# Performance work log

Hardware: AMD Instinct MI355X
Metric: run time of the kernel (lower is better)

## Reference

```python
import jax, jax.numpy as jnp
import numpy as np

N, D, E = 32768, 128, 524288
B, L = 64, 512          # 64 graphs of 512 nodes
H, DH = 8, 16           # heads, head dim


def setup_inputs() -> dict:
    key = jax.random.key(0)
    ks = jax.random.split(key, 16)
    s = 0.02
    w = lambda k, shape: (jax.random.normal(k, shape, jnp.float32) * s)
    z = lambda *shape: jnp.zeros(shape, jnp.float32)
    o = lambda *shape: jnp.ones(shape, jnp.float32)
    return {
        "x": jax.random.normal(ks[0], (N, D), jnp.float32),
        "edge_index": jax.random.randint(ks[1], (2, E), 0, N, jnp.int32),
        "eps": jnp.zeros(()),
        "W_loc1": w(ks[2], (D, 2 * D)), "b_loc1": z(2 * D),
        "W_loc2": w(ks[3], (2 * D, D)), "b_loc2": z(D),
        "g1": o(D), "beta1": z(D),
        "Wq": w(ks[4], (D, D)), "bq": z(D),
        "Wk": w(ks[5], (D, D)), "bk": z(D),
        "Wv": w(ks[6], (D, D)), "bv": z(D),
        "Wo": w(ks[7], (D, D)), "bo": z(D),
        "g2": o(D), "beta2": z(D),
        "Wf1": w(ks[8], (D, 2 * D)), "bf1": z(2 * D),
        "Wf2": w(ks[9], (2 * D, D)), "bf2": z(D),
        "g3": o(D), "beta3": z(D),
    }


def _bn(x, g, b):
    # BatchNorm1d, training mode: batch stats over the node dimension
    m = x.mean(0)
    v = x.var(0)
    return (x - m) * jax.lax.rsqrt(v + 1e-5) * g + b


def reference(x, edge_index, eps, W_loc1, b_loc1, W_loc2, b_loc2, g1, beta1,
              Wq, bq, Wk, bk, Wv, bv, Wo, bo, g2, beta2,
              Wf1, bf1, Wf2, bf2, g3, beta3):
    src, dst = edge_index[0], edge_index[1]
    # --- local MPNN (GIN): sum-aggregate neighbours then MLP ---
    agg = jax.ops.segment_sum(x[src], dst, num_segments=N)          # [N, D]
    h = (1.0 + eps) * x + agg
    h = jax.nn.relu(h @ W_loc1 + b_loc1) @ W_loc2 + b_loc2
    h_local = _bn(x + h, g1, beta1)
    # --- global attention over each graph's (permuted) node sequence ---
    xd = x.reshape(B, L, D)
    q = (xd @ Wq + bq).reshape(B, L, H, DH)
    k = (xd @ Wk + bk).reshape(B, L, H, DH)
    v = (xd @ Wv + bv).reshape(B, L, H, DH)
    scores = jnp.einsum("blhd,bmhd->bhlm", q, k) / np.sqrt(DH)
    attn = jax.nn.softmax(scores, axis=-1)
    o = jnp.einsum("bhlm,bmhd->blhd", attn, v).reshape(B, L, D)
    o = (o @ Wo + bo).reshape(N, D)
    h_attn = _bn(x + o, g2, beta2)
    # --- combine + FFN block ---
    h = h_local + h_attn
    f = jax.nn.relu(h @ Wf1 + bf1) @ Wf2 + bf2
    return _bn(h + f, g3, beta3)
```

## Files before the change

### kernel.cpp

```cpp
#include <hip/hip_runtime.h>
#include <cstdint>
#include <cstddef>

typedef unsigned short u16;
typedef unsigned int u32;

using short8 = __attribute__((ext_vector_type(8))) short;
using f32x4  = __attribute__((ext_vector_type(4))) float;

__device__ __forceinline__ float b2f(u16 v) {
  union { u32 u; float f; } c; c.u = ((u32)v) << 16; return c.f;
}
__device__ __forceinline__ u16 f2b(float f) {
  union { float f; u32 u; } c; c.f = f;
  u32 u = c.u;
  u += 0x7fffu + ((u >> 16) & 1u);
  return (u16)(u >> 16);
}

__global__ __launch_bounds__(256)
void f2bf_kernel(const float* __restrict__ in, u16* __restrict__ outp) {
  int i = blockIdx.x * 256 + threadIdx.x;
  int el = i * 2;
  int m = ((el >> 11) << 4) | ((el >> 5) & 15);
  int n = (((el >> 9) & 3) << 5) | (el & 31);
  float2 v = *(const float2*)(in + (size_t)m * 128 + n);
  *(u32*)(outp + el) = (u32)f2b(v.x) | ((u32)f2b(v.y) << 16);
}

__global__ __launch_bounds__(256)
void prep_kernel(const float* __restrict__ Wl1, const float* __restrict__ Wl2,
                 const float* __restrict__ Wq,  const float* __restrict__ Wk,
                 const float* __restrict__ Wv,  const float* __restrict__ Wo,
                 const float* __restrict__ Wf1, const float* __restrict__ Wf2,
                 const float* __restrict__ bl1, const float* __restrict__ bl2,
                 const float* __restrict__ bq,  const float* __restrict__ bk,
                 const float* __restrict__ bv,  const float* __restrict__ bo,
                 const float* __restrict__ bf1, const float* __restrict__ bf2,
                 u16* __restrict__ Bt, float* __restrict__ biasAll) {
  int idx = blockIdx.x * 256 + threadIdx.x;
  if (idx < 196608) {
    const float* W; int local, K, N;
    if      (idx <  32768) { W = Wl1; local = idx;          K = 128; N = 256; }
    else if (idx <  65536) { W = Wl2; local = idx - 32768;  K = 256; N = 128; }
    else if (idx <  81920) { W = Wq;  local = idx - 65536;  K = 128; N = 128; }
    else if (idx <  98304) { W = Wk;  local = idx - 81920;  K = 128; N = 128; }
    else if (idx < 114688) { W = Wv;  local = idx - 98304;  K = 128; N = 128; }
    else if (idx < 131072) { W = Wo;  local = idx - 114688; K = 128; N = 128; }
    else if (idx < 163840) { W = Wf1; local = idx - 131072; K = 128; N = 256; }
    else                   { W = Wf2; local = idx - 163840; K = 256; N = 128; }
    int ks2 = (K == 256) ? 3 : 2;
    int tile = local >> 9, within = local & 511;
    int nr = within >> 5, kc = within & 31;
    int n = ((tile >> ks2) << 4) + nr;
    int k = ((tile & ((1 << ks2) - 1)) << 5) + kc;
    Bt[idx] = f2b(W[(size_t)k * N + n]);
  }
  int t = idx - 196608;
  if (t >= 0 && t < 1280) {
    float v;
    if      (t <  256) v = bl1[t];
    else if (t <  384) v = bl2[t - 256];
    else if (t <  512) v = bq[t - 384];
    else if (t <  640) v = bk[t - 512];
    else if (t <  768) v = bv[t - 640];
    else if (t <  896) v = bo[t - 768];
    else if (t < 1152) v = bf1[t - 896];
    else               v = bf2[t - 1152];
    biasAll[t] = v;
  }
}

__global__ void hist_kernel(const int* __restrict__ dst, int* __restrict__ deg, int E) {
  int i = blockIdx.x * 256 + threadIdx.x;
  if (i < E) atomicAdd(&deg[dst[i]], 1);
}

__global__ __launch_bounds__(256)
void scan1_kernel(const int* __restrict__ deg, int* __restrict__ bsum) {
  int t = threadIdx.x, b = blockIdx.x;
  int v = deg[b * 256 + t];
#pragma unroll
  for (int off = 1; off < 64; off <<= 1) v += __shfl_xor(v, off);
  __shared__ int wsum[4];
  if ((t & 63) == 0) wsum[t >> 6] = v;
  __syncthreads();
  if (t == 0) bsum[b] = wsum[0] + wsum[1] + wsum[2] + wsum[3];
}

__global__ void scan2_kernel(const int* __restrict__ bsum, int* __restrict__ boff,
                             int* __restrict__ rowptrN) {
  __shared__ int sh[128];
  int t = threadIdx.x;
  int v = bsum[t];
  sh[t] = v;
  __syncthreads();
  for (int off = 1; off < 128; off <<= 1) {
    int u = (t >= off) ? sh[t - off] : 0;
    __syncthreads();
    sh[t] += u;
    __syncthreads();
  }
  boff[t] = sh[t] - v;
  if (t == 127) *rowptrN = sh[127];
}

__global__ __launch_bounds__(256)
void scan3_kernel(const int* __restrict__ deg, const int* __restrict__ boff,
                  int* __restrict__ rowptr, int* __restrict__ cursor) {
  __shared__ int sh[256];
  int t = threadIdx.x, b = blockIdx.x;
  int idx = b * 256 + t;
  int v = deg[idx];
  sh[t] = v;
  __syncthreads();
  for (int off = 1; off < 256; off <<= 1) {
    int u = (t >= off) ? sh[t - off] : 0;
    __syncthreads();
    sh[t] += u;
    __syncthreads();
  }
  int ex = sh[t] - v + boff[b];
  rowptr[idx] = ex;
  cursor[idx] = ex;
}

__global__ void scatter_kernel(const int* __restrict__ src, const int* __restrict__ dst,
                               int* __restrict__ cursor, int* __restrict__ csr, int E) {
  int i = blockIdx.x * 256 + threadIdx.x;
  if (i < E) {
    int d = dst[i];
    int pos = atomicAdd(&cursor[d], 1);
    csr[pos] = src[i];
  }
}

__global__ __launch_bounds__(256)
void agg_kernel(const u16* __restrict__ xb, const float* __restrict__ x,
                const int* __restrict__ csr, const int* __restrict__ rowptr,
                const float* __restrict__ eps, u16* __restrict__ hin, int N) {
  int node = blockIdx.x * 4 + (threadIdx.x >> 6);
  if (node >= N) return;
  int lane = threadIdx.x & 63;
  int laneoff = (lane >> 4) * 512 + (lane & 15) * 2;
  float ep1 = 1.0f + eps[0];
  int s0 = rowptr[node], s1 = rowptr[node + 1];
  float a0 = 0.f, a1 = 0.f;
  int e = s0;
  for (; e + 4 <= s1; e += 4) {
    int i0 = csr[e], i1 = csr[e + 1], i2 = csr[e + 2], i3 = csr[e + 3];
    u32 w0 = *(const u32*)(xb + (size_t)(i0 >> 4) * 2048 + (i0 & 15) * 32 + laneoff);
    u32 w1 = *(const u32*)(xb + (size_t)(i1 >> 4) * 2048 + (i1 & 15) * 32 + laneoff);
    u32 w2 = *(const u32*)(xb + (size_t)(i2 >> 4) * 2048 + (i2 & 15) * 32 + laneoff);
    u32 w3 = *(const u32*)(xb + (size_t)(i3 >> 4) * 2048 + (i3 & 15) * 32 + laneoff);
    a0 += b2f((u16)w0) + b2f((u16)w1) + b2f((u16)w2) + b2f((u16)w3);
    a1 += b2f((u16)(w0 >> 16)) + b2f((u16)(w1 >> 16))
        + b2f((u16)(w2 >> 16)) + b2f((u16)(w3 >> 16));
  }
  for (; e < s1; e++) {
    int s = csr[e];
    u32 w = *(const u32*)(xb + (size_t)(s >> 4) * 2048 + (s & 15) * 32 + laneoff);
    a0 += b2f((u16)w);
    a1 += b2f((u16)(w >> 16));
  }
  float2 xw = *(const float2*)(x + (size_t)node * 128 + lane * 2);
  a0 += ep1 * xw.x;
  a1 += ep1 * xw.y;
  *(u32*)(hin + (size_t)(node >> 4) * 2048 + (node & 15) * 32 + laneoff)
      = (u32)f2b(a0) | ((u32)f2b(a1) << 16);
}

template<int K>
__global__ __launch_bounds__(256)
void gemm_fast(const u16* __restrict__ A, const u16* __restrict__ Bt,
               const float* __restrict__ bias, const u16* __restrict__ residb,
               u16* __restrict__ C0, u16* __restrict__ C1, u16* __restrict__ C2,
               float* __restrict__ ssum, float* __restrict__ ssq,
               int ntshift, int relu, float scale0, int headmajor) {
  const int tid = threadIdx.x, wave = tid >> 6, lane = tid & 63;
  const int quad = lane >> 4, c = lane & 15;
  const int y = blockIdx.y;
  const int ti = y >> ntshift, ntv = y & ((1 << ntshift) - 1);
  const int Nout = 32 << ntshift;
  const int nc32 = Nout >> 5;
  constexpr int KT = K >> 5;
  const u16* Btp = Bt + (size_t)ti * Nout * K;
  const float* bp = bias + ti * Nout;
  u16* C = (ti == 0) ? C0 : ((ti == 1) ? C1 : C2);
  const float scl = (ti == 0) ? scale0 : 1.0f;
  const int row0 = blockIdx.x * 128 + wave * 32;
  const int mt0 = row0 >> 4;
  const int col0 = ntv * 32;
  const int loff = c * 32 + quad * 8;

  const u16* Ap0 = A   + (size_t)(mt0)     * KT * 512 + loff;
  const u16* Ap1 = A   + (size_t)(mt0 + 1) * KT * 512 + loff;
  const u16* Bp0 = Btp + (size_t)(ntv * 2)     * KT * 512 + loff;
  const u16* Bp1 = Btp + (size_t)(ntv * 2 + 1) * KT * 512 + loff;

  f32x4 acc[2][2];
#pragma unroll
  for (int i = 0; i < 2; i++)
#pragma unroll
    for (int j = 0; j < 2; j++)
#pragma unroll
      for (int r = 0; r < 4; r++) acc[i][j][r] = 0.f;

#pragma unroll
  for (int i = 0; i < KT; i++) {
    short8 a0 = *(const short8*)(Ap0 + i * 512);
    short8 a1 = *(const short8*)(Ap1 + i * 512);
    short8 b0 = *(const short8*)(Bp0 + i * 512);
    short8 b1 = *(const short8*)(Bp1 + i * 512);
    acc[0][0] = __builtin_amdgcn_mfma_f32_16x16x32_bf16(a0, b0, acc[0][0], 0, 0, 0);
    acc[0][1] = __builtin_amdgcn_mfma_f32_16x16x32_bf16(a0, b1, acc[0][1], 0, 0, 0);
    acc[1][0] = __builtin_amdgcn_mfma_f32_16x16x32_bf16(a1, b0, acc[1][0], 0, 0, 0);
    acc[1][1] = __builtin_amdgcn_mfma_f32_16x16x32_bf16(a1, b1, acc[1][1], 0, 0, 0);
  }

#pragma unroll
  for (int ci = 0; ci < 2; ci++) {
    int col = col0 + ci * 16 + c;
    float bv = bp[col];
    float sp = 0.f, qp = 0.f;
#pragma unroll
    for (int mi = 0; mi < 2; mi++) {
#pragma unroll
      for (int r = 0; r < 4; r++) {
        int m = row0 + mi * 16 + quad * 4 + r;
        float v = acc[mi][ci][r] + bv;
        if (relu) v = fmaxf(v, 0.f);
        if (residb)
          v += b2f(residb[((size_t)(mt0 + mi) * 4 + (col >> 5)) * 512
                          + (quad * 4 + r) * 32 + (col & 31)]);
        v *= scl;
        size_t cidx;
        if (headmajor) {
          int bb = m >> 9, j = m & 511;
          cidx = (size_t)(bb * 8 + (col >> 4)) * 8192 + (size_t)j * 16 + (col & 15);
        } else {
          cidx = ((size_t)(mt0 + mi) * nc32 + ntv) * 512
               + (quad * 4 + r) * 32 + ci * 16 + c;
        }
        C[cidx] = f2b(v);
        sp += v; qp += v * v;
      }
    }
    if (ssum) {
      sp += __shfl_xor(sp, 16); sp += __shfl_xor(sp, 32);
      qp += __shfl_xor(qp, 16); qp += __shfl_xor(qp, 32);
      if (quad == 0) {
        atomicAdd(&ssum[col], sp);
        atomicAdd(&ssq[col], qp);
      }
    }
  }
}

__global__ __launch_bounds__(512)
void attn_kernel(const u16* __restrict__ Q, const u16* __restrict__ Km,
                 const u16* __restrict__ Vm, u16* __restrict__ O) {
  __shared__ __align__(16) u16 Vt[16 * 520];
  __shared__ __align__(16) u16 Psh[8][16 * 40];
  const int bh = blockIdx.x >> 1, qhalf = blockIdx.x & 1;
  const int b = bh >> 3, hh = bh & 7;
  const size_t qkvbase = (size_t)bh * 8192;
  const int tid = threadIdx.x;

  {
    int g = tid >> 5, i = (tid >> 1) & 15, dh = tid & 1;
    int jA = g * 32 + i;
    const u16* vp = Vm + qkvbase + (size_t)jA * 16 + dh * 8;
    short8 rowA = *(const short8*)(vp);
    short8 rowB = *(const short8*)(vp + 256);
    int j2 = g * 32 + 2 * i;
#pragma unroll
    for (int d = 0; d < 8; d++)
      *(u32*)&Vt[(dh * 8 + d) * 520 + j2] =
          (u32)(u16)rowA[d] | ((u32)(u16)rowB[d] << 16);
  }
  __syncthreads();

  const int wave = tid >> 6, lane = tid & 63;
  const int quad = lane >> 4, c = lane & 15;
  u16* Pw = &Psh[wave][0];
  u32* Pw32 = (u32*)Pw;

  short8 ones;
#pragma unroll
  for (int i = 0; i < 8; i++) ones[i] = (short)0x3F80;
  const f32x4 zero = {0.f, 0.f, 0.f, 0.f};

  short8 qf[2] = {(short8)0, (short8)0};
#pragma unroll
  for (int t = 0; t < 2; t++) {
    int qt = qhalf * 16 + wave + t * 8;
    if (quad < 2)
      qf[t] = *(const short8*)(Q + qkvbase + (size_t)(qt * 16 + c) * 16 + quad * 8);
  }

#pragma unroll
  for (int t = 0; t < 2; t++) {
    const int qt = qhalf * 16 + wave + t * 8;
    f32x4 accO = zero, accL = zero;
#pragma unroll 4
    for (int jp = 0; jp < 16; jp++) {
      short8 kf0 = (short8)0, kf1 = (short8)0;
      if (quad < 2) {
        kf0 = *(const short8*)(Km + qkvbase + (size_t)(jp * 32 + c) * 16 + quad * 8);
        kf1 = *(const short8*)(Km + qkvbase + (size_t)(jp * 32 + 16 + c) * 16 + quad * 8);
      }
      f32x4 s0 = __builtin_amdgcn_mfma_f32_16x16x32_bf16(qf[t], kf0, zero, 0, 0, 0);
      f32x4 s1 = __builtin_amdgcn_mfma_f32_16x16x32_bf16(qf[t], kf1, zero, 0, 0, 0);
#pragma unroll
      for (int r = 0; r < 4; r++) {
        union { float f; u32 u; } u0, u1;
        u0.f = exp2f(s0[r]);
        u1.f = exp2f(s1[r]);
        Pw32[(quad * 4 + r) * 20 + c] = (u0.u >> 16) | (u1.u & 0xffff0000u);
      }
      short8 pf = *(const short8*)&Pw[c * 40 + quad * 8];
      short8 vf = *(const short8*)&Vt[c * 520 + jp * 32 + quad * 8];
      accO = __builtin_amdgcn_mfma_f32_16x16x32_bf16(pf, vf, accO, 0, 0, 0);
      accL = __builtin_amdgcn_mfma_f32_16x16x32_bf16(pf, ones, accL, 0, 0, 0);
    }
#pragma unroll
    for (int r = 0; r < 4; r++) {
      float o = accO[r] / accL[r];
      size_t oidx = ((size_t)(b * 32 + qt) * 4 + (hh >> 1)) * 512
                  + (quad * 4 + r) * 32 + (hh & 1) * 16 + c;
      O[oidx] = f2b(o);
    }
  }
}

__global__ __launch_bounds__(256)
void combine_kernel(const u16* __restrict__ y1, const u16* __restrict__ y2,
                    const float* __restrict__ stats,
                    const float* __restrict__ g1, const float* __restrict__ be1,
                    const float* __restrict__ g2, const float* __restrict__ be2,
                    u16* __restrict__ hout, float invM) {
  int i = blockIdx.x * 256 + threadIdx.x;
  int e0 = i * 2;
  int c = (((e0 >> 9) & 3) << 5) | (e0 & 31);
  float sc1a, sh1a, sc1b, sh1b, sc2a, sh2a, sc2b, sh2b;
  {
    float m = stats[c] * invM, vv = stats[128 + c] * invM - m * m;
    sc1a = g1[c] * rsqrtf(vv + 1e-5f); sh1a = be1[c] - m * sc1a;
    m = stats[c + 1] * invM; vv = stats[129 + c] * invM - m * m;
    sc1b = g1[c + 1] * rsqrtf(vv + 1e-5f); sh1b = be1[c + 1] - m * sc1b;
    m = stats[256 + c] * invM; vv = stats[384 + c] * invM - m * m;
    sc2a = g2[c] * rsqrtf(vv + 1e-5f); sh2a = be2[c] - m * sc2a;
    m = stats[257 + c] * invM; vv = stats[385 + c] * invM - m * m;
    sc2b = g2[c + 1] * rsqrtf(vv + 1e-5f); sh2b = be2[c + 1] - m * sc2b;
  }
  u32 w1 = *(const u32*)(y1 + e0);
  u32 w2 = *(const u32*)(y2 + e0);
  float r0 = b2f((u16)w1) * sc1a + sh1a + b2f((u16)w2) * sc2a + sh2a;
  float r1 = b2f((u16)(w1 >> 16)) * sc1b + sh1b + b2f((u16)(w2 >> 16)) * sc2b + sh2b;
  *(u32*)(hout + e0) = (u32)f2b(r0) | ((u32)f2b(r1) << 16);
}

__global__ __launch_bounds__(256)
void norm_kernel(const u16* __restrict__ y3, const float* __restrict__ stats3,
                 const float* __restrict__ g3, const float* __restrict__ be3,
                 float* __restrict__ outp, float invM) {
  int i = blockIdx.x * 256 + threadIdx.x;
  int e0 = i * 2;
  int m = ((e0 >> 11) << 4) | ((e0 >> 5) & 15);
  int c = (((e0 >> 9) & 3) << 5) | (e0 & 31);
  float mm = stats3[c] * invM, vv = stats3[128 + c] * invM - mm * mm;
  float sca = g3[c] * rsqrtf(vv + 1e-5f), sha = be3[c] - mm * sca;
  mm = stats3[c + 1] * invM; vv = stats3[129 + c] * invM - mm * mm;
  float scb = g3[c + 1] * rsqrtf(vv + 1e-5f), shb = be3[c + 1] - mm * scb;
  u32 w = *(const u32*)(y3 + e0);
  float2 r;
  r.x = b2f((u16)w) * sca + sha;
  r.y = b2f((u16)(w >> 16)) * scb + shb;
  *(float2*)(outp + (size_t)m * 128 + c) = r;
}

extern "C" void kernel_launch(void* const* d_in, const int* in_sizes, int n_in,
                              void* d_out, int out_size, void* d_ws, size_t ws_size,
                              hipStream_t stream) {
  const float* x   = (const float*)d_in[0];
  const int*   ei  = (const int*)d_in[1];
  const float* eps = (const float*)d_in[2];
  const float* Wl1 = (const float*)d_in[3];  const float* bl1 = (const float*)d_in[4];
  const float* Wl2 = (const float*)d_in[5];  const float* bl2 = (const float*)d_in[6];
  const float* g1  = (const float*)d_in[7];  const float* be1 = (const float*)d_in[8];
  const float* Wq  = (const float*)d_in[9];  const float* bq  = (const float*)d_in[10];
  const float* Wk  = (const float*)d_in[11]; const float* bk  = (const float*)d_in[12];
  const float* Wv  = (const float*)d_in[13]; const float* bv  = (const float*)d_in[14];
  const float* Wo  = (const float*)d_in[15]; const float* bo  = (const float*)d_in[16];
  const float* g2  = (const float*)d_in[17]; const float* be2 = (const float*)d_in[18];
  const float* Wf1 = (const float*)d_in[19]; const float* bf1 = (const float*)d_in[20];
  const float* Wf2 = (const float*)d_in[21]; const float* bf2 = (const float*)d_in[22];
  const float* g3  = (const float*)d_in[23]; const float* be3 = (const float*)d_in[24];
  float* out = (float*)d_out;

  const int N = in_sizes[0] / 128;
  const int E = in_sizes[1] / 2;
  const size_t MB = 1048576;
  const float invM = 1.0f / (float)N;

  char* ws = (char*)d_ws;
  u16* hin = (u16*)(ws + 0);
  u16* t1  = (u16*)(ws + 8 * MB);
  int* deg    = (int*)(ws + 8 * MB);
  int* rowptr = (int*)(ws + 8 * MB + 256 * 1024);
  int* cursor = (int*)(ws + 8 * MB + 512 * 1024);
  int* csr    = (int*)(ws + 8 * MB + 768 * 1024);
  u16* qb  = (u16*)(ws + 24 * MB);
  u16* kb  = (u16*)(ws + 32 * MB);
  u16* vb  = (u16*)(ws + 40 * MB);
  u16* xb  = (u16*)(ws + 48 * MB);
  u16* y2  = xb;
  float* stats = (float*)(ws + 56 * MB);
  int* bsum = (int*)(ws + 56 * MB + 8192);
  int* boff = (int*)(ws + 56 * MB + 8192 + 512);
  u16* y1 = (u16*)d_out;
  u16*   BtAll   = (u16*)((char*)d_out + 8 * MB);
  float* biasAll = (float*)((char*)d_out + 8 * MB + 400 * 1024);

  hipMemsetAsync(deg, 0, (size_t)N * sizeof(int), stream);
  hipMemsetAsync(stats, 0, 6 * 128 * sizeof(float), stream);

  const int* srcv = ei;
  const int* dstv = ei + E;
  const float QSCL = 0.25f * 1.44269504088896f;

  prep_kernel<<<774, 256, 0, stream>>>(Wl1, Wl2, Wq, Wk, Wv, Wo, Wf1, Wf2,
                                       bl1, bl2, bq, bk, bv, bo, bf1, bf2,
                                       BtAll, biasAll);
  f2bf_kernel<<<(N * 128 / 2) / 256, 256, 0, stream>>>(x, xb);
  hist_kernel<<<(E + 255) / 256, 256, 0, stream>>>(dstv, deg, E);
  scan1_kernel<<<N / 256, 256, 0, stream>>>(deg, bsum);
  scan2_kernel<<<1, 128, 0, stream>>>(bsum, boff, rowptr + N);
  scan3_kernel<<<N / 256, 256, 0, stream>>>(deg, boff, rowptr, cursor);
  scatter_kernel<<<(E + 255) / 256, 256, 0, stream>>>(srcv, dstv, cursor, csr, E);
  agg_kernel<<<N / 4, 256, 0, stream>>>(xb, x, csr, rowptr, eps, hin, N);

  dim3 blk(256);
  gemm_fast<128><<<dim3(N / 128, 8), blk, 0, stream>>>(hin, BtAll + 0, biasAll + 0,
      nullptr, t1, nullptr, nullptr, nullptr, nullptr, 3, 1, 1.0f, 0);
  gemm_fast<256><<<dim3(N / 128, 4), blk, 0, stream>>>(t1, BtAll + 32768, biasAll + 256,
      xb, y1, nullptr, nullptr, stats + 0, stats + 128, 2, 0, 1.0f, 0);
  gemm_fast<128><<<dim3(N / 128, 12), blk, 0, stream>>>(xb, BtAll + 65536, biasAll + 384,
      nullptr, qb, kb, vb, nullptr, nullptr, 2, 0, QSCL, 1);
  attn_kernel<<<(N / 512) * 8 * 2, dim3(512), 0, stream>>>(qb, kb, vb, hin);
  gemm_fast<128><<<dim3(N / 128, 4), blk, 0, stream>>>(hin, BtAll + 114688, biasAll + 768,
      xb, y2, nullptr, nullptr, stats + 256, stats + 384, 2, 0, 1.0f, 0);
  combine_kernel<<<(N * 128 / 2) / 256, blk, 0, stream>>>(y1, y2, stats,
      g1, be1, g2, be2, qb, invM);
  gemm_fast<128><<<dim3(N / 128, 8), blk, 0, stream>>>(qb, BtAll + 131072, biasAll + 896,
      nullptr, t1, nullptr, nullptr, nullptr, nullptr, 3, 1, 1.0f, 0);
  gemm_fast<256><<<dim3(N / 128, 4), blk, 0, stream>>>(t1, BtAll + 163840, biasAll + 1152,
      qb, kb, nullptr, nullptr, stats + 512, stats + 640, 2, 0, 1.0f, 0);
  norm_kernel<<<(N * 128 / 2) / 256, blk, 0, stream>>>(kb, stats + 512, g3, be3, out, invM);
}
```

Measured before the change: 427.6 us.

## Merge prologue kernels, fuse first GEMM with QKV projection, widen attention blocks

Three prologue kernels (weight prep, x to bf16, degree histogram) become one launch split by block range. The first local-MLP GEMM and the QKV projection GEMM are merged into one grid, since both take K=128 and do not depend on each other. The attention kernel now covers all 32 query tiles per block instead of splitting into two halves, so each K/V load is reused by four query tiles, at the cost of half as many blocks and more registers. The generic GEMM loses its multi-output and head-major paths, and bf16 packing in attention uses a byte permute instruction.

Measured after the change: 413.2 us. -3.4%, faster.

```diff
diff --git a/kernel.cpp b/kernel.cpp
--- a/kernel.cpp
+++ b/kernel.cpp
@@ -19,61 +19,61 @@
 }
 
 __global__ __launch_bounds__(256)
-void f2bf_kernel(const float* __restrict__ in, u16* __restrict__ outp) {
-  int i = blockIdx.x * 256 + threadIdx.x;
-  int el = i * 2;
-  int m = ((el >> 11) << 4) | ((el >> 5) & 15);
-  int n = (((el >> 9) & 3) << 5) | (el & 31);
-  float2 v = *(const float2*)(in + (size_t)m * 128 + n);
-  *(u32*)(outp + el) = (u32)f2b(v.x) | ((u32)f2b(v.y) << 16);
-}
-
-__global__ __launch_bounds__(256)
-void prep_kernel(const float* __restrict__ Wl1, const float* __restrict__ Wl2,
-                 const float* __restrict__ Wq,  const float* __restrict__ Wk,
-                 const float* __restrict__ Wv,  const float* __restrict__ Wo,
-                 const float* __restrict__ Wf1, const float* __restrict__ Wf2,
-                 const float* __restrict__ bl1, const float* __restrict__ bl2,
-                 const float* __restrict__ bq,  const float* __restrict__ bk,
-                 const float* __restrict__ bv,  const float* __restrict__ bo,
-                 const float* __restrict__ bf1, const float* __restrict__ bf2,
-                 u16* __restrict__ Bt, float* __restrict__ biasAll) {
-  int idx = blockIdx.x * 256 + threadIdx.x;
-  if (idx < 196608) {
-    const float* W; int local, K, N;
-    if      (idx <  32768) { W = Wl1; local = idx;          K = 128; N = 256; }
-    else if (idx <  65536) { W = Wl2; local = idx - 32768;  K = 256; N = 128; }
-    else if (idx <  81920) { W = Wq;  local = idx - 65536;  K = 128; N = 128; }
-    else if (idx <  98304) { W = Wk;  local = idx - 81920;  K = 128; N = 128; }
-    else if (idx < 114688) { W = Wv;  local = idx - 98304;  K = 128; N = 128; }
-    else if (idx < 131072) { W = Wo;  local = idx - 114688; K = 128; N = 128; }
-    else if (idx < 163840) { W = Wf1; local = idx - 131072; K = 128; N = 256; }
-    else                   { W = Wf2; local = idx - 163840; K = 256; N = 128; }
-    int ks2 = (K == 256) ? 3 : 2;
-    int tile = local >> 9, within = local & 511;
-    int nr = within >> 5, kc = within & 31;
-    int n = ((tile >> ks2) << 4) + nr;
-    int k = ((tile & ((1 << ks2) - 1)) << 5) + kc;
-    Bt[idx] = f2b(W[(size_t)k * N + n]);
-  }
-  int t = idx - 196608;
-  if (t >= 0 && t < 1280) {
-    float v;
-    if      (t <  256) v = bl1[t];
-    else if (t <  384) v = bl2[t - 256];
-    else if (t <  512) v = bq[t - 384];
-    else if (t <  640) v = bk[t - 512];
-    else if (t <  768) v = bv[t - 640];
-    else if (t <  896) v = bo[t - 768];
-    else if (t < 1152) v = bf1[t - 896];
-    else               v = bf2[t - 1152];
-    biasAll[t] = v;
-  }
-}
-
-__global__ void hist_kernel(const int* __restrict__ dst, int* __restrict__ deg, int E) {
-  int i = blockIdx.x * 256 + threadIdx.x;
-  if (i < E) atomicAdd(&deg[dst[i]], 1);
+void prologue_kernel(const float* __restrict__ Wl1, const float* __restrict__ Wl2,
+                     const float* __restrict__ Wq,  const float* __restrict__ Wk,
+                     const float* __restrict__ Wv,  const float* __restrict__ Wo,
+                     const float* __restrict__ Wf1, const float* __restrict__ Wf2,
+                     const float* __restrict__ bl1, const float* __restrict__ bl2,
+                     const float* __restrict__ bq,  const float* __restrict__ bk,
+                     const float* __restrict__ bv,  const float* __restrict__ bo,
+                     const float* __restrict__ bf1, const float* __restrict__ bf2,
+                     u16* __restrict__ Bt, float* __restrict__ biasAll,
+                     const float* __restrict__ x, u16* __restrict__ xb,
+                     const int* __restrict__ dstv, int* __restrict__ deg, int E) {
+  int bid = blockIdx.x;
+  if (bid < 774) {
+    int idx = bid * 256 + threadIdx.x;
+    if (idx < 196608) {
+      const float* W; int local, K, N;
+      if      (idx <  32768) { W = Wl1; local = idx;          K = 128; N = 256; }
+      else if (idx <  65536) { W = Wl2; local = idx - 32768;  K = 256; N = 128; }
+      else if (idx <  81920) { W = Wq;  local = idx - 65536;  K = 128; N = 128; }
+      else if (idx <  98304) { W = Wk;  local = idx - 81920;  K = 128; N = 128; }
+      else if (idx < 114688) { W = Wv;  local = idx - 98304;  K = 128; N = 128; }
+      else if (idx < 131072) { W = Wo;  local = idx - 114688; K = 128; N = 128; }
+      else if (idx < 163840) { W = Wf1; local = idx - 131072; K = 128; N = 256; }
+      else                   { W = Wf2; local = idx - 163840; K = 256; N = 128; }
+      int ks2 = (K == 256) ? 3 : 2;
+      int tile = local >> 9, within = local & 511;
+      int nr = within >> 5, kc = within & 31;
+      int n = ((tile >> ks2) << 4) + nr;
+      int k = ((tile & ((1 << ks2) - 1)) << 5) + kc;
+      Bt[idx] = f2b(W[(size_t)k * N + n]);
+    }
+    int t = idx - 196608;
+    if (t >= 0 && t < 1280) {
+      float v;
+      if      (t <  256) v = bl1[t];
+      else if (t <  384) v = bl2[t - 256];
+      else if (t <  512) v = bq[t - 384];
+      else if (t <  640) v = bk[t - 512];
+      else if (t <  768) v = bv[t - 640];
+      else if (t <  896) v = bo[t - 768];
+      else if (t < 1152) v = bf1[t - 896];
+      else               v = bf2[t - 1152];
+      biasAll[t] = v;
+    }
+  } else if (bid < 774 + 8192) {
+    int i = (bid - 774) * 256 + threadIdx.x;
+    int el = i * 2;
+    int m = ((el >> 11) << 4) | ((el >> 5) & 15);
+    int n = (((el >> 9) & 3) << 5) | (el & 31);
+    float2 v = *(const float2*)(x + (size_t)m * 128 + n);
+    *(u32*)(xb + el) = (u32)f2b(v.x) | ((u32)f2b(v.y) << 16);
+  } else {
+    int i = (bid - 774 - 8192) * 256 + threadIdx.x;
+    if (i < E) atomicAdd(&deg[dstv[i]], 1);
+  }
 }
 
 __global__ __launch_bounds__(256)
@@ -174,29 +174,25 @@
 __global__ __launch_bounds__(256)
 void gemm_fast(const u16* __restrict__ A, const u16* __restrict__ Bt,
                const float* __restrict__ bias, const u16* __restrict__ residb,
-               u16* __restrict__ C0, u16* __restrict__ C1, u16* __restrict__ C2,
+               u16* __restrict__ C0,
                float* __restrict__ ssum, float* __restrict__ ssq,
-               int ntshift, int relu, float scale0, int headmajor) {
+               int ntshift, int relu) {
   const int tid = threadIdx.x, wave = tid >> 6, lane = tid & 63;
   const int quad = lane >> 4, c = lane & 15;
-  const int y = blockIdx.y;
-  const int ti = y >> ntshift, ntv = y & ((1 << ntshift) - 1);
-  const int Nout = 32 << ntshift;
-  const int nc32 = Nout >> 5;
+  const int ntv = blockIdx.y;
+  const int nc32 = 1 << ntshift;
   constexpr int KT = K >> 5;
-  const u16* Btp = Bt + (size_t)ti * Nout * K;
-  const float* bp = bias + ti * Nout;
-  u16* C = (ti == 0) ? C0 : ((ti == 1) ? C1 : C2);
-  const float scl = (ti == 0) ? scale0 : 1.0f;
+  const float* bp = bias;
+  u16* C = C0;
   const int row0 = blockIdx.x * 128 + wave * 32;
   const int mt0 = row0 >> 4;
   const int col0 = ntv * 32;
   const int loff = c * 32 + quad * 8;
 
-  const u16* Ap0 = A   + (size_t)(mt0)     * KT * 512 + loff;
-  const u16* Ap1 = A   + (size_t)(mt0 + 1) * KT * 512 + loff;
-  const u16* Bp0 = Btp + (size_t)(ntv * 2)     * KT * 512 + loff;
-  const u16* Bp1 = Btp + (size_t)(ntv * 2 + 1) * KT * 512 + loff;
+  const u16* Ap0 = A  + (size_t)(mt0)     * KT * 512 + loff;
+  const u16* Ap1 = A  + (size_t)(mt0 + 1) * KT * 512 + loff;
+  const u16* Bp0 = Bt + (size_t)(ntv * 2)     * KT * 512 + loff;
+  const u16* Bp1 = Bt + (size_t)(ntv * 2 + 1) * KT * 512 + loff;
 
   f32x4 acc[2][2];
 #pragma unroll
@@ -227,12 +223,90 @@
     for (int mi = 0; mi < 2; mi++) {
 #pragma unroll
       for (int r = 0; r < 4; r++) {
-        int m = row0 + mi * 16 + quad * 4 + r;
         float v = acc[mi][ci][r] + bv;
         if (relu) v = fmaxf(v, 0.f);
         if (residb)
           v += b2f(residb[((size_t)(mt0 + mi) * 4 + (col >> 5)) * 512
                           + (quad * 4 + r) * 32 + (col & 31)]);
+        size_t cidx = ((size_t)(mt0 + mi) * nc32 + ntv) * 512
+                    + (quad * 4 + r) * 32 + ci * 16 + c;
+        C[cidx] = f2b(v);
+        sp += v; qp += v * v;
+      }
+    }
+    if (ssum) {
+      sp += __shfl_xor(sp, 16); sp += __shfl_xor(sp, 32);
+      qp += __shfl_xor(qp, 16); qp += __shfl_xor(qp, 32);
+      if (quad == 0) {
+        atomicAdd(&ssum[col], sp);
+        atomicAdd(&ssq[col], qp);
+      }
+    }
+  }
+}
+
+__global__ __launch_bounds__(256)
+void gemm_t1qkv(const u16* __restrict__ hin, const u16* __restrict__ xb,
+                const u16* __restrict__ BtAll, const float* __restrict__ biasAll,
+                u16* __restrict__ t1, u16* __restrict__ qb, u16* __restrict__ kb,
+                u16* __restrict__ vb, float qscl) {
+  const int tid = threadIdx.x, wave = tid >> 6, lane = tid & 63;
+  const int quad = lane >> 4, c = lane & 15;
+  const int y = blockIdx.y;
+  const u16* A; const u16* Btp; const float* bp; u16* C;
+  int ntv, nc32, relu, headmajor; float scl;
+  if (y < 8) {
+    A = hin; Btp = BtAll; bp = biasAll; C = t1;
+    ntv = y; nc32 = 8; relu = 1; headmajor = 0; scl = 1.0f;
+  } else {
+    int y2 = y - 8, ti = y2 >> 2;
+    ntv = y2 & 3; A = xb;
+    Btp = BtAll + 65536 + ti * 16384;
+    bp = biasAll + 384 + ti * 128;
+    C = (ti == 0) ? qb : ((ti == 1) ? kb : vb);
+    nc32 = 4; relu = 0; headmajor = 1; scl = (ti == 0) ? qscl : 1.0f;
+  }
+  const int row0 = blockIdx.x * 128 + wave * 32;
+  const int mt0 = row0 >> 4;
+  const int col0 = ntv * 32;
+  const int loff = c * 32 + quad * 8;
+
+  const u16* Ap0 = A   + (size_t)(mt0)     * 4 * 512 + loff;
+  const u16* Ap1 = A   + (size_t)(mt0 + 1) * 4 * 512 + loff;
+  const u16* Bp0 = Btp + (size_t)(ntv * 2)     * 4 * 512 + loff;
+  const u16* Bp1 = Btp + (size_t)(ntv * 2 + 1) * 4 * 512 + loff;
+
+  f32x4 acc[2][2];
+#pragma unroll
+  for (int i = 0; i < 2; i++)
+#pragma unroll
+    for (int j = 0; j < 2; j++)
+#pragma unroll
+      for (int r = 0; r < 4; r++) acc[i][j][r] = 0.f;
+
+#pragma unroll
+  for (int i = 0; i < 4; i++) {
+    short8 a0 = *(const short8*)(Ap0 + i * 512);
+    short8 a1 = *(const short8*)(Ap1 + i * 512);
+    short8 b0 = *(const short8*)(Bp0 + i * 512);
+    short8 b1 = *(const short8*)(Bp1 + i * 512);
+    acc[0][0] = __builtin_amdgcn_mfma_f32_16x16x32_bf16(a0, b0, acc[0][0], 0, 0, 0);
+    acc[0][1] = __builtin_amdgcn_mfma_f32_16x16x32_bf16(a0, b1, acc[0][1], 0, 0, 0);
+    acc[1][0] = __builtin_amdgcn_mfma_f32_16x16x32_bf16(a1, b0, acc[1][0], 0, 0, 0);
+    acc[1][1] = __builtin_amdgcn_mfma_f32_16x16x32_bf16(a1, b1, acc[1][1], 0, 0, 0);
+  }
+
+#pragma unroll
+  for (int ci = 0; ci < 2; ci++) {
+    int col = col0 + ci * 16 + c;
+    float bv = bp[col];
+#pragma unroll
+    for (int mi = 0; mi < 2; mi++) {
+#pragma unroll
+      for (int r = 0; r < 4; r++) {
+        int m = row0 + mi * 16 + quad * 4 + r;
+        float v = acc[mi][ci][r] + bv;
+        if (relu) v = fmaxf(v, 0.f);
         v *= scl;
         size_t cidx;
         if (headmajor) {
@@ -243,15 +317,6 @@
                + (quad * 4 + r) * 32 + ci * 16 + c;
         }
         C[cidx] = f2b(v);
-        sp += v; qp += v * v;
-      }
-    }
-    if (ssum) {
-      sp += __shfl_xor(sp, 16); sp += __shfl_xor(sp, 32);
-      qp += __shfl_xor(qp, 16); qp += __shfl_xor(qp, 32);
-      if (quad == 0) {
-        atomicAdd(&ssum[col], sp);
-        atomicAdd(&ssq[col], qp);
       }
     }
   }
@@ -262,7 +327,7 @@
                  const u16* __restrict__ Vm, u16* __restrict__ O) {
   __shared__ __align__(16) u16 Vt[16 * 520];
   __shared__ __align__(16) u16 Psh[8][16 * 40];
-  const int bh = blockIdx.x >> 1, qhalf = blockIdx.x & 1;
+  const int bh = blockIdx.x;
   const int b = bh >> 3, hh = bh & 7;
   const size_t qkvbase = (size_t)bh * 8192;
   const int tid = threadIdx.x;
@@ -291,25 +356,26 @@
   for (int i = 0; i < 8; i++) ones[i] = (short)0x3F80;
   const f32x4 zero = {0.f, 0.f, 0.f, 0.f};
 
-  short8 qf[2] = {(short8)0, (short8)0};
-#pragma unroll
-  for (int t = 0; t < 2; t++) {
-    int qt = qhalf * 16 + wave + t * 8;
+  short8 qf[4];
+  f32x4 accO[4], accL[4];
+#pragma unroll
+  for (int t = 0; t < 4; t++) {
+    qf[t] = (short8)0;
+    accO[t] = zero; accL[t] = zero;
+    int qt = wave + t * 8;
     if (quad < 2)
       qf[t] = *(const short8*)(Q + qkvbase + (size_t)(qt * 16 + c) * 16 + quad * 8);
   }
 
-#pragma unroll
-  for (int t = 0; t < 2; t++) {
-    const int qt = qhalf * 16 + wave + t * 8;
-    f32x4 accO = zero, accL = zero;
-#pragma unroll 4
-    for (int jp = 0; jp < 16; jp++) {
-      short8 kf0 = (short8)0, kf1 = (short8)0;
-      if (quad < 2) {
-        kf0 = *(const short8*)(Km + qkvbase + (size_t)(jp * 32 + c) * 16 + quad * 8);
-        kf1 = *(const short8*)(Km + qkvbase + (size_t)(jp * 32 + 16 + c) * 16 + quad * 8);
-      }
+  for (int jp = 0; jp < 16; jp++) {
+    short8 kf0 = (short8)0, kf1 = (short8)0;
+    if (quad < 2) {
+      kf0 = *(const short8*)(Km + qkvbase + (size_t)(jp * 32 + c) * 16 + quad * 8);
+      kf1 = *(const short8*)(Km + qkvbase + (size_t)(jp * 32 + 16 + c) * 16 + quad * 8);
+    }
+    short8 vf = *(const short8*)&Vt[c * 520 + jp * 32 + quad * 8];
+#pragma unroll
+    for (int t = 0; t < 4; t++) {
       f32x4 s0 = __builtin_amdgcn_mfma_f32_16x16x32_bf16(qf[t], kf0, zero, 0, 0, 0);
       f32x4 s1 = __builtin_amdgcn_mfma_f32_16x16x32_bf16(qf[t], kf1, zero, 0, 0, 0);
 #pragma unroll
@@ -317,16 +383,19 @@
         union { float f; u32 u; } u0, u1;
         u0.f = exp2f(s0[r]);
         u1.f = exp2f(s1[r]);
-        Pw32[(quad * 4 + r) * 20 + c] = (u0.u >> 16) | (u1.u & 0xffff0000u);
+        Pw32[(quad * 4 + r) * 20 + c] = __builtin_amdgcn_perm(u1.u, u0.u, 0x07060302u);
       }
       short8 pf = *(const short8*)&Pw[c * 40 + quad * 8];
-      short8 vf = *(const short8*)&Vt[c * 520 + jp * 32 + quad * 8];
-      accO = __builtin_amdgcn_mfma_f32_16x16x32_bf16(pf, vf, accO, 0, 0, 0);
-      accL = __builtin_amdgcn_mfma_f32_16x16x32_bf16(pf, ones, accL, 0, 0, 0);
-    }
+      accO[t] = __builtin_amdgcn_mfma_f32_16x16x32_bf16(pf, vf, accO[t], 0, 0, 0);
+      accL[t] = __builtin_amdgcn_mfma_f32_16x16x32_bf16(pf, ones, accL[t], 0, 0, 0);
+    }
+  }
+#pragma unroll
+  for (int t = 0; t < 4; t++) {
+    int qt = wave + t * 8;
 #pragma unroll
     for (int r = 0; r < 4; r++) {
-      float o = accO[r] / accL[r];
+      float o = accO[t][r] / accL[t][r];
       size_t oidx = ((size_t)(b * 32 + qt) * 4 + (hh >> 1)) * 512
                   + (quad * 4 + r) * 32 + (hh & 1) * 16 + c;
       O[oidx] = f2b(o);
@@ -430,11 +499,10 @@
   const int* dstv = ei + E;
   const float QSCL = 0.25f * 1.44269504088896f;
 
-  prep_kernel<<<774, 256, 0, stream>>>(Wl1, Wl2, Wq, Wk, Wv, Wo, Wf1, Wf2,
-                                       bl1, bl2, bq, bk, bv, bo, bf1, bf2,
-                                       BtAll, biasAll);
-  f2bf_kernel<<<(N * 128 / 2) / 256, 256, 0, stream>>>(x, xb);
-  hist_kernel<<<(E + 255) / 256, 256, 0, stream>>>(dstv, deg, E);
+  prologue_kernel<<<774 + 8192 + 2048, 256, 0, stream>>>(
+      Wl1, Wl2, Wq, Wk, Wv, Wo, Wf1, Wf2,
+      bl1, bl2, bq, bk, bv, bo, bf1, bf2,
+      BtAll, biasAll, x, xb, dstv, deg, E);
   scan1_kernel<<<N / 256, 256, 0, stream>>>(deg, bsum);
   scan2_kernel<<<1, 128, 0, stream>>>(bsum, boff, rowptr + N);
   scan3_kernel<<<N / 256, 256, 0, stream>>>(deg, boff, rowptr, cursor);
@@ -442,20 +510,18 @@
   agg_kernel<<<N / 4, 256, 0, stream>>>(xb, x, csr, rowptr, eps, hin, N);
 
   dim3 blk(256);
-  gemm_fast<128><<<dim3(N / 128, 8), blk, 0, stream>>>(hin, BtAll + 0, biasAll + 0,
-      nullptr, t1, nullptr, nullptr, nullptr, nullptr, 3, 1, 1.0f, 0);
+  gemm_t1qkv<<<dim3(N / 128, 20), blk, 0, stream>>>(hin, xb, BtAll, biasAll,
+                                                    t1, qb, kb, vb, QSCL);
   gemm_fast<256><<<dim3(N / 128, 4), blk, 0, stream>>>(t1, BtAll + 32768, biasAll + 256,
-      xb, y1, nullptr, nullptr, stats + 0, stats + 128, 2, 0, 1.0f, 0);
-  gemm_fast<128><<<dim3(N / 128, 12), blk, 0, stream>>>(xb, BtAll + 65536, biasAll + 384,
-      nullptr, qb, kb, vb, nullptr, nullptr, 2, 0, QSCL, 1);
-  attn_kernel<<<(N / 512) * 8 * 2, dim3(512), 0, stream>>>(qb, kb, vb, hin);
+      xb, y1, stats + 0, stats + 128, 2, 0);
+  attn_kernel<<<(N / 512) * 8, dim3(512), 0, stream>>>(qb, kb, vb, hin);
   gemm_fast<128><<<dim3(N / 128, 4), blk, 0, stream>>>(hin, BtAll + 114688, biasAll + 768,
-      xb, y2, nullptr, nullptr, stats + 256, stats + 384, 2, 0, 1.0f, 0);
+      xb, y2, stats + 256, stats + 384, 2, 0);
   combine_kernel<<<(N * 128 / 2) / 256, blk, 0, stream>>>(y1, y2, stats,
       g1, be1, g2, be2, qb, invM);
   gemm_fast<128><<<dim3(N / 128, 8), blk, 0, stream>>>(qb, BtAll + 131072, biasAll + 896,
-      nullptr, t1, nullptr, nullptr, nullptr, nullptr, 3, 1, 1.0f, 0);
+      nullptr, t1, nullptr, nullptr, 3, 1);
   gemm_fast<256><<<dim3(N / 128, 4), blk, 0, stream>>>(t1, BtAll + 163840, biasAll + 1152,
-      qb, kb, nullptr, nullptr, stats + 512, stats + 640, 2, 0, 1.0f, 0);
+      qb, kb, stats + 512, stats + 640, 2, 0);
   norm_kernel<<<(N * 128 / 2) / 256, blk, 0, stream>>>(kb, stats + 512, g3, be3, out, invM);
 }
```
